# Kernel tuning notes

Measured on AMD Instinct MI355X. Metric: run time of the kernel, lower is better.

The kernel has to match this reference:

```python
import jax, jax.numpy as jnp
import numpy as np

S, B, D, E2 = 2048, 32, 1024, 1024  # src_len, batch, dec_hid_dim, 2*enc_hid_dim


def setup_inputs() -> dict:
    key = jax.random.key(0)
    k1, k2, k3, k4, k5 = jax.random.split(key, 5)
    scale = 1.0 / np.sqrt(D)
    return {
        "dec_prev_hidden": jax.random.normal(k1, (B, D), dtype=jnp.float32),
        "enc_outputs": jax.random.normal(k2, (S, B, E2), dtype=jnp.float32),
        "Wb": jax.random.normal(k3, (D, D), dtype=jnp.float32) * scale,
        "Wc": jax.random.normal(k4, (D, E2), dtype=jnp.float32) * scale,
        "Wa": jax.random.normal(k5, (D,), dtype=jnp.float32) * scale,
    }


def reference(dec_prev_hidden, enc_outputs, Wb, Wc, Wa):
    # weighted_s_t_1: [B, D] broadcast over seq axis; weighted_H: [S, B, D]
    weighted_s = jnp.einsum('bd,ed->be', dec_prev_hidden, Wb)          # [B, D]
    weighted_H = jnp.einsum('sbe,de->sbd', enc_outputs, Wc)            # [S, B, D]
    score = jnp.einsum('sbd,d->sb', jnp.tanh(weighted_H + weighted_s), Wa)  # [S, B]
    # torch F.softmax with no dim on a 3-D tensor -> dim=0 (seq axis)
    attn = jax.nn.softmax(score, axis=0)                               # [S, B]
    # bmm([B,1,S], [B,S,2E]) -> [B,1,2E], then permute -> [1,B,2E]
    context = jnp.einsum('sb,sbe->be', attn, enc_outputs)              # [B, 2E]
    return context[None, :, :]                                         # [1, B, 2E]
```

## Files before the change

### kernel.cpp

```cpp
#include <hip/hip_runtime.h>
#include <hip/hip_bf16.h>
#include <stdint.h>

#define S_LEN 2048
#define BATCH 32
#define MROWS (S_LEN*BATCH)

typedef __attribute__((ext_vector_type(8))) short bf16x8;
typedef __attribute__((ext_vector_type(4))) float f32x4;
typedef unsigned short ushort_t;

__device__ inline unsigned int pk2bf(float a, float b) {
  float2 t; t.x = a; t.y = b;
  __hip_bfloat162 h = __float22bfloat162_rn(t);
  union { __hip_bfloat162 h; unsigned int u; } c; c.h = h;
  return c.u;
}

__device__ inline float bflo(unsigned int u) { return __uint_as_float(u << 16); }
__device__ inline float bfhi(unsigned int u) { return __uint_as_float(u & 0xffff0000u); }

__device__ inline void gload_lds16(const void* g, void* l) {
  __builtin_amdgcn_global_load_lds(
      (const __attribute__((address_space(1))) unsigned int*)g,
      (__attribute__((address_space(3))) unsigned int*)l, 16, 0, 0);
}

__device__ inline float fast_tanh(float x) {
  float e = __expf(2.0f * x);
  return 1.0f - 2.0f / (e + 1.0f);
}

__global__ __launch_bounds__(256) void conv_enc_kernel(
    const float4* __restrict__ in, uint4* __restrict__ outp)
{
  const size_t j0 = (size_t)blockIdx.x * 2048 + threadIdx.x;
  float4 a[8], b[8];
  #pragma unroll
  for (int k = 0; k < 8; ++k) {
    const size_t j = j0 + (size_t)k * 256;
    a[k] = in[j * 2];
    b[k] = in[j * 2 + 1];
  }
  #pragma unroll
  for (int k = 0; k < 8; ++k) {
    uint4 w;
    w.x = pk2bf(a[k].x, a[k].y); w.y = pk2bf(a[k].z, a[k].w);
    w.z = pk2bf(b[k].x, b[k].y); w.w = pk2bf(b[k].z, b[k].w);
    outp[j0 + (size_t)k * 256] = w;
  }
}

__global__ __launch_bounds__(256) void prep_small_kernel(
    const float* __restrict__ dec, const float* __restrict__ Wb,
    const float* __restrict__ Wc, ushort_t* __restrict__ WcBf,
    float* __restrict__ wsum)
{
  const int t = threadIdx.x;
  const int bid = blockIdx.x;
  if (bid < 64) {
    const int base = bid * 16384;
    for (int i = 0; i < 16; ++i) {
      int idx = base + i * 1024 + t * 4;
      float4 v = *(const float4*)(Wc + idx);
      uint2 w; w.x = pk2bf(v.x, v.y); w.y = pk2bf(v.z, v.w);
      *(uint2*)(WcBf + idx) = w;
    }
  } else {
    const int j = bid - 64;
    __shared__ float sdec[32][65];
    __shared__ float swb[32][65];
    const int b = t & 31, nl = t >> 5;
    float acc0 = 0.f, acc1 = 0.f, acc2 = 0.f, acc3 = 0.f;
    for (int c = 0; c < 16; ++c) {
      __syncthreads();
      for (int idx = t; idx < 2048; idx += 256) {
        int rr = idx >> 6, dd = idx & 63;
        sdec[rr][dd] = dec[rr * 1024 + c * 64 + dd];
        swb[rr][dd]  = Wb[(size_t)(j * 32 + rr) * 1024 + c * 64 + dd];
      }
      __syncthreads();
      #pragma unroll 8
      for (int dd = 0; dd < 64; ++dd) {
        float dv = sdec[b][dd];
        acc0 += dv * swb[nl][dd];
        acc1 += dv * swb[nl + 8][dd];
        acc2 += dv * swb[nl + 16][dd];
        acc3 += dv * swb[nl + 24][dd];
      }
    }
    wsum[b * 1024 + j * 32 + nl]      = acc0;
    wsum[b * 1024 + j * 32 + nl + 8]  = acc1;
    wsum[b * 1024 + j * 32 + nl + 16] = acc2;
    wsum[b * 1024 + j * 32 + nl + 24] = acc3;
  }
}

__global__ __launch_bounds__(256, 4) void score_kernel(
    const ushort_t* __restrict__ encBf, const ushort_t* __restrict__ WcBf,
    const float* __restrict__ wsum, const float* __restrict__ Wa,
    float* __restrict__ scoreP8)
{
  __shared__ ushort_t Ab[128][64];
  __shared__ ushort_t Bb[128][64];
  __shared__ float scorep[128];

  const int tid = threadIdx.x;
  const int lane = tid & 63;
  const int l15 = lane & 15, q = lane >> 4;
  const int r7 = l15 & 7;
  const int wid = tid >> 6;
  const int wr = wid >> 1, wc = wid & 1;
  const int bid = blockIdx.x;
  const int mi = bid & 15, nblk = (bid >> 4) & 7, mg = bid >> 7;
  const size_t rowBase = (size_t)(mg * 16 + mi) * 128;

  if (tid < 128) scorep[tid] = 0.f;

  int aOff[4], bOff[4], dOff[4];
  #pragma unroll
  for (int k = 0; k < 4; ++k) {
    const int s = k * 256 + tid;
    const int r = s >> 3, c = s & 7;
    const int swz = (c ^ (r & 7)) * 8;
    aOff[k] = (int)(r * 1024 + swz);
    bOff[k] = (int)((nblk * 128 + r) * 1024 + swz);
    dOff[k] = s * 8;
  }
  const ushort_t* aBase = encBf + rowBase * 1024;
  ushort_t* const aL = &Ab[0][0];
  ushort_t* const bL = &Bb[0][0];

  int aRow[4], bRow[4];
  #pragma unroll
  for (int m = 0; m < 4; ++m) aRow[m] = (wr * 64 + m * 16 + l15) * 64;
  #pragma unroll
  for (int n = 0; n < 4; ++n) bRow[n] = (wc * 64 + n * 16 + l15) * 64;
  const int ch0 = (q ^ r7) * 8;
  const int ch1 = ((4 + q) ^ r7) * 8;

  f32x4 acc[4][4];
  #pragma unroll
  for (int m = 0; m < 4; ++m)
    #pragma unroll
    for (int n = 0; n < 4; ++n) { f32x4 z = {0.f,0.f,0.f,0.f}; acc[m][n] = z; }

  for (int kt = 0; kt < 16; ++kt) {
    const int ko = kt * 64;
    #pragma unroll
    for (int k = 0; k < 4; ++k) {
      gload_lds16(aBase + ko + aOff[k], aL + dOff[k]);
      gload_lds16(WcBf + ko + bOff[k], bL + dOff[k]);
    }
    __syncthreads();

    #pragma unroll
    for (int kk = 0; kk < 2; ++kk) {
      const int cho = kk ? ch1 : ch0;
      bf16x8 af[4], bv[4];
      #pragma unroll
      for (int m = 0; m < 4; ++m) af[m] = *(const bf16x8*)(aL + aRow[m] + cho);
      #pragma unroll
      for (int n = 0; n < 4; ++n) bv[n] = *(const bf16x8*)(bL + bRow[n] + cho);
      #pragma unroll
      for (int m = 0; m < 4; ++m)
        #pragma unroll
        for (int n = 0; n < 4; ++n)
          acc[m][n] = __builtin_amdgcn_mfma_f32_16x16x32_bf16(
              af[m], bv[n], acc[m][n], 0, 0, 0);
    }
    __syncthreads();
  }

  #pragma unroll
  for (int m = 0; m < 4; ++m) {
    #pragma unroll
    for (int i = 0; i < 4; ++i) {
      const int rowl = wr * 64 + m * 16 + q * 4 + i;
      const int bb2 = rowl & 31;
      float v = 0.f;
      #pragma unroll
      for (int n = 0; n < 4; ++n) {
        const int col = nblk * 128 + wc * 64 + n * 16 + l15;
        float x = acc[m][n][i] + wsum[bb2 * 1024 + col];
        v += fast_tanh(x) * Wa[col];
      }
      v += __shfl_xor(v, 1); v += __shfl_xor(v, 2);
      v += __shfl_xor(v, 4); v += __shfl_xor(v, 8);
      if (l15 == 0) atomicAdd(&scorep[rowl], v);
    }
  }
  __syncthreads();
  if (tid < 128) scoreP8[(rowBase + tid) * 8 + nblk] = scorep[tid];
}

__global__ __launch_bounds__(256) void ctx_kernel(
    const ushort_t* __restrict__ encBf, const float* __restrict__ scoreP8,
    float* __restrict__ out)
{
  const int b = blockIdx.x & 31, sc = blockIdx.x >> 5;
  const int t = threadIdx.x;
  __shared__ float eCh[128];
  __shared__ float red[256];

  const int chunk0 = sc * 128;
  float ssum = 0.f;
  for (int s = t; s < S_LEN; s += 256) {
    const float4* p = (const float4*)(scoreP8 + ((size_t)s * 32 + b) * 8);
    float4 u = p[0], v = p[1];
    float scv = ((u.x + u.y) + (u.z + u.w)) + ((v.x + v.y) + (v.z + v.w));
    float e = __expf(scv);
    ssum += e;
    const int d = s - chunk0;
    if ((unsigned)d < 128u) eCh[d] = e;
  }
  red[t] = ssum;
  __syncthreads();
  #pragma unroll
  for (int o = 128; o > 0; o >>= 1) {
    if (t < o) red[t] += red[t + o];
    __syncthreads();
  }
  const float inv = 1.0f / red[0];

  float a0 = 0.f, a1 = 0.f, a2 = 0.f, a3 = 0.f;
  const int e0 = t * 4;
  #pragma unroll 4
  for (int si = 0; si < 128; ++si) {
    const int s = chunk0 + si;
    const float a = eCh[si];
    uint2 w = *(const uint2*)(encBf + ((size_t)s * 32 + b) * 1024 + e0);
    a0 += a * bflo(w.x); a1 += a * bfhi(w.x);
    a2 += a * bflo(w.y); a3 += a * bfhi(w.y);
  }
  float* op = out + b * 1024 + e0;
  atomicAdd(op + 0, a0 * inv); atomicAdd(op + 1, a1 * inv);
  atomicAdd(op + 2, a2 * inv); atomicAdd(op + 3, a3 * inv);
}

extern "C" void kernel_launch(void* const* d_in, const int* in_sizes, int n_in,
                              void* d_out, int out_size, void* d_ws, size_t ws_size,
                              hipStream_t stream) {
  const float* dec = (const float*)d_in[0];
  const float* enc = (const float*)d_in[1];
  const float* Wb  = (const float*)d_in[2];
  const float* Wc  = (const float*)d_in[3];
  const float* Wa  = (const float*)d_in[4];
  float* out = (float*)d_out;
  (void)in_sizes; (void)n_in; (void)ws_size;

  char* ws = (char*)d_ws;
  ushort_t* encBf   = (ushort_t*)ws;
  ushort_t* WcBf    = (ushort_t*)(ws + 134217728);
  float*    wsum    = (float*)(ws + 134217728 + 2097152);
  float*    scoreP8 = (float*)(ws + 134217728 + 2097152 + 131072);

  hipMemsetAsync(out, 0, (size_t)out_size * sizeof(float), stream);
  prep_small_kernel<<<96, 256, 0, stream>>>(dec, Wb, Wc, WcBf, wsum);
  conv_enc_kernel<<<4096, 256, 0, stream>>>((const float4*)enc, (uint4*)encBf);
  score_kernel<<<4096, 256, 0, stream>>>(encBf, WcBf, wsum, Wa, scoreP8);
  ctx_kernel<<<512, 256, 0, stream>>>(encBf, scoreP8, out);
}
```

Baseline: 388.5 us.

## Fuse fp32-to-bf16 encoder conversion into score GEMM A-tile loading

```diff
diff --git a/kernel.cpp b/kernel.cpp
--- a/kernel.cpp
+++ b/kernel.cpp
@@ -29,26 +29,6 @@
 __device__ inline float fast_tanh(float x) {
   float e = __expf(2.0f * x);
   return 1.0f - 2.0f / (e + 1.0f);
-}
-
-__global__ __launch_bounds__(256) void conv_enc_kernel(
-    const float4* __restrict__ in, uint4* __restrict__ outp)
-{
-  const size_t j0 = (size_t)blockIdx.x * 2048 + threadIdx.x;
-  float4 a[8], b[8];
-  #pragma unroll
-  for (int k = 0; k < 8; ++k) {
-    const size_t j = j0 + (size_t)k * 256;
-    a[k] = in[j * 2];
-    b[k] = in[j * 2 + 1];
-  }
-  #pragma unroll
-  for (int k = 0; k < 8; ++k) {
-    uint4 w;
-    w.x = pk2bf(a[k].x, a[k].y); w.y = pk2bf(a[k].z, a[k].w);
-    w.z = pk2bf(b[k].x, b[k].y); w.w = pk2bf(b[k].z, b[k].w);
-    outp[j0 + (size_t)k * 256] = w;
-  }
 }
 
 __global__ __launch_bounds__(256) void prep_small_kernel(
@@ -97,9 +77,9 @@
 }
 
 __global__ __launch_bounds__(256, 4) void score_kernel(
-    const ushort_t* __restrict__ encBf, const ushort_t* __restrict__ WcBf,
-    const float* __restrict__ wsum, const float* __restrict__ Wa,
-    float* __restrict__ scoreP8)
+    const float4* __restrict__ encF4, ushort_t* __restrict__ encBf,
+    const ushort_t* __restrict__ WcBf, const float* __restrict__ wsum,
+    const float* __restrict__ Wa, float* __restrict__ scoreP8)
 {
   __shared__ ushort_t Ab[128][64];
   __shared__ ushort_t Bb[128][64];
@@ -117,17 +97,18 @@
 
   if (tid < 128) scorep[tid] = 0.f;
 
-  int aOff[4], bOff[4], dOff[4];
+  const int tRow = tid >> 4;
+  const int f4 = tid & 15;
+  const int swzT = (((f4 >> 1) ^ (tRow & 7)) * 8) + ((f4 & 1) * 4);
+
+  int bOff[4], dOff[4];
   #pragma unroll
   for (int k = 0; k < 4; ++k) {
     const int s = k * 256 + tid;
     const int r = s >> 3, c = s & 7;
-    const int swz = (c ^ (r & 7)) * 8;
-    aOff[k] = (int)(r * 1024 + swz);
-    bOff[k] = (int)((nblk * 128 + r) * 1024 + swz);
+    bOff[k] = (int)((nblk * 128 + r) * 1024 + ((c ^ (r & 7)) * 8));
     dOff[k] = s * 8;
   }
-  const ushort_t* aBase = encBf + rowBase * 1024;
   ushort_t* const aL = &Ab[0][0];
   ushort_t* const bL = &Bb[0][0];
 
@@ -148,9 +129,23 @@
   for (int kt = 0; kt < 16; ++kt) {
     const int ko = kt * 64;
     #pragma unroll
-    for (int k = 0; k < 4; ++k) {
-      gload_lds16(aBase + ko + aOff[k], aL + dOff[k]);
+    for (int k = 0; k < 4; ++k)
       gload_lds16(WcBf + ko + bOff[k], bL + dOff[k]);
+
+    float4 av[8];
+    #pragma unroll
+    for (int k = 0; k < 8; ++k)
+      av[k] = encF4[(rowBase + k * 16 + tRow) * 256 + kt * 16 + f4];
+
+    #pragma unroll
+    for (int k = 0; k < 8; ++k) {
+      uint2 w;
+      w.x = pk2bf(av[k].x, av[k].y);
+      w.y = pk2bf(av[k].z, av[k].w);
+      const int r = k * 16 + tRow;
+      *(uint2*)(aL + r * 64 + swzT) = w;
+      if (nblk == 0)
+        *(uint2*)(encBf + (rowBase + r) * 1024 + ko + f4 * 4) = w;
     }
     __syncthreads();
 
@@ -257,7 +252,7 @@
 
   hipMemsetAsync(out, 0, (size_t)out_size * sizeof(float), stream);
   prep_small_kernel<<<96, 256, 0, stream>>>(dec, Wb, Wc, WcBf, wsum);
-  conv_enc_kernel<<<4096, 256, 0, stream>>>((const float4*)enc, (uint4*)encBf);
-  score_kernel<<<4096, 256, 0, stream>>>(encBf, WcBf, wsum, Wa, scoreP8);
+  score_kernel<<<4096, 256, 0, stream>>>((const float4*)enc, encBf, WcBf,
+                                         wsum, Wa, scoreP8);
   ctx_kernel<<<512, 256, 0, stream>>>(encBf, scoreP8, out);
 }
```

Result: faster. 378.6 us (-2.6%).
